# Performance work log

Measured on AMD Instinct MI355X. Metric: run time of the kernel, lower is better.

## Reference

```python
import jax, jax.numpy as jnp
import numpy as np

B, C, H, W = 8, 256, 64, 64
NH, FF, L, K = 8, 1024, 3, 64
THR = 0.5
DH = C // NH
SCALE = 1.0 / float(np.sqrt(DH))
N = H * W


def setup_inputs() -> dict:
    key = jax.random.key(0)
    ks = jax.random.split(key, 16)
    s = 0.02
    rn = lambda k, shape: (jax.random.normal(k, shape, jnp.float32) * s)
    return {
        "x": jax.random.normal(ks[0], (B, C, H, W), jnp.float32),
        "y": jax.random.normal(ks[1], (B, C, H, W), jnp.float32),
        "proj_w": rn(ks[2], (C, 2 * C)), "proj_b": rn(ks[3], (C,)),
        "sal_w": rn(ks[4], (1, C)), "sal_b": rn(ks[5], (1,)),
        "soft_w": rn(ks[6], (2, K, C)), "soft_b": rn(ks[7], (2, K)),
        "attn_in_w": rn(ks[8], (2, L, 3 * C, C)), "attn_in_b": rn(ks[9], (2, L, 3 * C)),
        "attn_out_w": rn(ks[10], (2, L, C, C)), "attn_out_b": rn(ks[11], (2, L, C)),
        "n1_g": jnp.ones((2, L, C), jnp.float32), "n1_b": jnp.zeros((2, L, C), jnp.float32),
        "ffn_w1": rn(ks[12], (2, L, FF, C)), "ffn_b1": rn(ks[13], (2, L, FF)),
        "ffn_w2": rn(ks[14], (2, L, C, FF)), "ffn_b2": rn(ks[15], (2, L, C)),
        "n2_g": jnp.ones((2, L, C), jnp.float32), "n2_b": jnp.zeros((2, L, C), jnp.float32),
    }


def _ln(t, g, b, eps=1e-5):
    m = t.mean(-1, keepdims=True)
    v = ((t - m) ** 2).mean(-1, keepdims=True)
    return (t - m) / jnp.sqrt(v + eps) * g + b


def _layers(q, kv, p, side):
    # q: [B,N,C] pixel queries, kv: [B,K,C] soft-pooled tokens
    for l in range(L):
        iw, ib = p["attn_in_w"][side, l], p["attn_in_b"][side, l]
        qq = (q @ iw[:C].T + ib[:C]).reshape(B, -1, NH, DH)
        kk = (kv @ iw[C:2 * C].T + ib[C:2 * C]).reshape(B, K, NH, DH)
        vv = (kv @ iw[2 * C:].T + ib[2 * C:]).reshape(B, K, NH, DH)
        att = jax.nn.softmax(jnp.einsum('bnhd,bkhd->bhnk', qq, kk) * SCALE, axis=-1)
        o = jnp.einsum('bhnk,bkhd->bnhd', att, vv).reshape(B, -1, C)
        o = o @ p["attn_out_w"][side, l].T + p["attn_out_b"][side, l]
        q = _ln(q + o, p["n1_g"][side, l], p["n1_b"][side, l])
        h = jax.nn.relu(q @ p["ffn_w1"][side, l].T + p["ffn_b1"][side, l])
        h = h @ p["ffn_w2"][side, l].T + p["ffn_b2"][side, l]
        q = _ln(q + h, p["n2_g"][side, l], p["n2_b"][side, l])
    return q


def _forward(x, y, proj_w, proj_b, sal_w, sal_b, soft_w, soft_b,
             attn_in_w, attn_in_b, attn_out_w, attn_out_b, n1_g, n1_b,
             ffn_w1, ffn_b1, ffn_w2, ffn_b2, n2_g, n2_b):
    p = dict(attn_in_w=attn_in_w, attn_in_b=attn_in_b, attn_out_w=attn_out_w,
             attn_out_b=attn_out_b, n1_g=n1_g, n1_b=n1_b, ffn_w1=ffn_w1,
             ffn_b1=ffn_b1, ffn_w2=ffn_w2, ffn_b2=ffn_b2, n2_g=n2_g, n2_b=n2_b)
    xc = jnp.concatenate([x, y], axis=1)                                  # [B,2C,H,W]
    feat = jnp.einsum('oc,bchw->bohw', proj_w, xc) + proj_b[None, :, None, None]
    sal = jnp.einsum('oc,bchw->bohw', sal_w, feat) + sal_b[None, :, None, None]  # [B,1,H,W]
    heat = jax.nn.sigmoid(sal)
    fg_mask = (heat >= THR).reshape(B, 1, N)
    bg_mask = (heat < 1.0 - THR).reshape(B, 1, N)
    fmap = feat.reshape(B, C, N)
    q0 = fmap.transpose(0, 2, 1)                                          # [B,N,C]
    out = fmap
    for side, hm in ((0, heat), (1, 1.0 - heat)):
        wf = feat * hm                                                    # [B,C,H,W]
        sw = (jnp.einsum('kc,bchw->bkhw', soft_w[side], wf)
              + soft_b[side][None, :, None, None]).reshape(B, K, N)       # [B,K,N]
        pool = jnp.einsum('bkn,bcn->bkc', sw, wf.reshape(B, C, N))        # [B,K,C]
        qs = _layers(q0, pool, p, side)                                   # [B,N,C]
        mask = fg_mask if side == 0 else bg_mask
        out = jnp.where(mask, qs.transpose(0, 2, 1), out)
    # per-image skip: if no fg or no bg pixels, keep original feature
    valid = fg_mask.any(axis=(1, 2)) & bg_mask.any(axis=(1, 2))           # [B]
    out = jnp.where(valid[:, None, None], out, fmap)
    return out.reshape(B, C, H, W)


def reference(x, y, proj_w, proj_b, sal_w, sal_b, soft_w, soft_b,
              attn_in_w, attn_in_b, attn_out_w, attn_out_b, n1_g, n1_b,
              ffn_w1, ffn_b1, ffn_w2, ffn_b2, n2_g, n2_b):
    return _forward(x, y, proj_w, proj_b, sal_w, sal_b, soft_w, soft_b,
                    attn_in_w, attn_in_b, attn_out_w, attn_out_b, n1_g, n1_b,
                    ffn_w1, ffn_b1, ffn_w2, ffn_b2, n2_g, n2_b)
```

## Files before the change

kernel.cpp:

```cpp
#include <hip/hip_runtime.h>
#include <stdint.h>

#define B_ 8
#define C_ 256
#define N_ 4096
#define K_ 64
#define NH_ 8
#define FF_ 1024
#define L_ 3
#define M_ (B_*N_)
#define SCALE_ 0.17677669529663687f

typedef float f32x4 __attribute__((ext_vector_type(4)));
typedef __bf16 v8bf __attribute__((ext_vector_type(8)));

__device__ __forceinline__ float b2f(unsigned short h){
  union { uint32_t u; float f; } v; v.u = ((uint32_t)h) << 16; return v.f;
}
__device__ __forceinline__ unsigned short f2b(float f){
  union { float f; uint32_t u; } v; v.f = f;
  uint32_t r = v.u + 0x7fffu + ((v.u >> 16) & 1u);
  return (unsigned short)(r >> 16);
}
__device__ __forceinline__ void gload_lds16(const void* g, void* l){
  __builtin_amdgcn_global_load_lds(
      (const __attribute__((address_space(1))) unsigned int*)g,
      (__attribute__((address_space(3))) unsigned int*)l, 16, 0, 0);
}
__device__ __forceinline__ void unpack8(uint4 v, float* o){
  o[0]=b2f((unsigned short)(v.x & 0xffff)); o[1]=b2f((unsigned short)(v.x >> 16));
  o[2]=b2f((unsigned short)(v.y & 0xffff)); o[3]=b2f((unsigned short)(v.y >> 16));
  o[4]=b2f((unsigned short)(v.z & 0xffff)); o[5]=b2f((unsigned short)(v.z >> 16));
  o[6]=b2f((unsigned short)(v.w & 0xffff)); o[7]=b2f((unsigned short)(v.w >> 16));
}

__global__ __launch_bounds__(256) void k_f32_to_bf16(const float* __restrict__ src,
                                                     unsigned short* __restrict__ dst, int n){
  int i4 = (blockIdx.x*256 + threadIdx.x)*4;
  if (i4 >= n) return;
  float4 v = *(const float4*)(src + i4);
  uint32_t p0 = (uint32_t)f2b(v.x) | ((uint32_t)f2b(v.y) << 16);
  uint32_t p1 = (uint32_t)f2b(v.z) | ((uint32_t)f2b(v.w) << 16);
  *(uint2*)(dst + i4) = make_uint2(p0, p1);
}

__global__ __launch_bounds__(256) void k_build_xcT(const float* __restrict__ x,
                                                   const float* __restrict__ y,
                                                   unsigned short* __restrict__ xcT){
  __shared__ float t[32][33];
  int b = blockIdx.z;
  int n0 = blockIdx.x*32, c0 = blockIdx.y*32;
  int tx = threadIdx.x, ty = threadIdx.y;
  const float* src = (c0 < 256) ? (x + ((size_t)b*256 + c0)*N_)
                                : (y + ((size_t)b*256 + (c0-256))*N_);
  #pragma unroll
  for (int i = 0; i < 4; i++){
    int cl = ty*4 + i;
    t[cl][tx] = src[(size_t)cl*N_ + n0 + tx];
  }
  __syncthreads();
  #pragma unroll
  for (int i = 0; i < 4; i++){
    int nl = ty*4 + i;
    xcT[((size_t)b*N_ + n0 + nl)*512 + c0 + tx] = f2b(t[tx][nl]);
  }
}

__global__ __launch_bounds__(256) void k_featmir(const float* __restrict__ featT,
                                                 unsigned short* __restrict__ featbf,
                                                 unsigned short* __restrict__ featC){
  __shared__ float t[32][33];
  int b = blockIdx.z;
  int n0 = blockIdx.x*32, c0 = blockIdx.y*32;
  int tx = threadIdx.x, ty = threadIdx.y;
  #pragma unroll
  for (int i = 0; i < 4; i++){
    int nl = ty*4 + i;
    size_t m = (size_t)b*N_ + n0 + nl;
    float v = featT[m*256 + c0 + tx];
    t[nl][tx] = v;
    featbf[m*256 + c0 + tx] = f2b(v);
  }
  __syncthreads();
  #pragma unroll
  for (int i = 0; i < 4; i++){
    int cl = ty*4 + i;
    featC[((size_t)b*256 + c0 + cl)*(size_t)N_ + n0 + tx] = f2b(t[tx][cl]);
  }
}

__global__ __launch_bounds__(512) void k_compute_u(const float* __restrict__ sal_w,
                                                   const float* __restrict__ proj_w,
                                                   const float* __restrict__ proj_b,
                                                   const float* __restrict__ sal_b,
                                                   double* __restrict__ u){
  int c2 = threadIdx.x;
// ... 84 lines not shown
      v8bf af[4], bfr[4];
      #pragma unroll
      for (int f = 0; f < 4; f++){
        int ra = wr*64 + f*16 + lr;
        int rb2 = wc*64 + f*16 + lr;
        int u = kk*4 + lk;
        af[f]  = *(const v8bf*)(&ldsA[ra*64 + ((u ^ (ra&7))<<3)]);
        bfr[f] = *(const v8bf*)(&ldsB[rb2*64 + ((u ^ (rb2&7))<<3)]);
      }
      #pragma unroll
      for (int fi = 0; fi < 4; fi++)
        #pragma unroll
        for (int fj = 0; fj < 4; fj++)
          acc[fi][fj] = __builtin_amdgcn_mfma_f32_16x16x32_bf16(af[fi], bfr[fj], acc[fi][fj], 0, 0, 0);
    }
    __syncthreads();
  }
  if (EPI == 1 || EPI == 2){
    unsigned short* st = &smem[0][0][0];
    #pragma unroll
    for (int fj = 0; fj < 4; fj++){
      int col = wc*64 + fj*16 + lr;
      float bv = bias[n0 + col];
      #pragma unroll
      for (int fi = 0; fi < 4; fi++){
        int rl = wr*64 + fi*16 + lk*4;
        #pragma unroll
        for (int r = 0; r < 4; r++){
          float v = acc[fi][fj][r] + bv;
          if (EPI == 1) v = fmaxf(v, 0.f);
          st[(rl + r)*136 + col] = f2b(v);
        }
      }
    }
    __syncthreads();
    #pragma unroll
    for (int it = 0; it < 8; it++){
      int idx = it*256 + tid;
      int row = idx >> 4, c8 = (idx & 15)*8;
      *(uint4*)((unsigned short*)out + (size_t)(m0+row)*N + n0 + c8)
          = *(const uint4*)&st[row*136 + c8];
    }
  } else {
    #pragma unroll
    for (int fj = 0; fj < 4; fj++){
      int col = n0 + wc*64 + fj*16 + lr;
      float bv = bias[col];
      #pragma unroll
      for (int fi = 0; fi < 4; fi++){
        int rb = m0 + wr*64 + fi*16 + lk*4;
        #pragma unroll
        for (int r = 0; r < 4; r++){
          float v = acc[fi][fj][r] + bv;
          if (EPI == 3){
            int row = rb + r;
            ((unsigned short*)out)[((size_t)(row>>6)*256 + col)*64 + (row&63)] = f2b(v);
          } else {
            ((float*)out)[(size_t)(rb + r)*N + col] = v;
          }
        }
      }
    }
  }
}

__global__ __launch_bounds__(256) void k_kv(
    const unsigned short* __restrict__ pool, const unsigned short* __restrict__ iw,
    const float* __restrict__ ib, unsigned short* __restrict__ kk_bf,
    unsigned short* __restrict__ vvT_bf){
  __shared__ unsigned short smem[2][2][128*64];
  int tid = threadIdx.x;
  int w = tid >> 6, l = tid & 63;
  int m0 = blockIdx.x * 128, n0 = blockIdx.y * 128;
  int isv = blockIdx.z;
  const unsigned short* W = iw + (size_t)(isv ? 512 : 256)*256;
  const float* bias = ib + (isv ? 512 : 256);
  int wr = w >> 1, wc = w & 1;
  int lr = l & 15, lk = l >> 4;
  f32x4 acc[4][4] = {};
  #pragma unroll
  for (int i = 0; i < 4; i++){
    int idx = i*256 + tid;
    int row = idx >> 3, su = ((idx & 7) ^ (row & 7))*8;
    gload_lds16(pool + (size_t)(m0+row)*256 + su, &smem[0][0][idx*8]);
    gload_lds16(W + (size_t)(n0+row)*256 + su, &smem[0][1][idx*8]);
  }
  __syncthreads();
  for (int t = 0; t < 4; ++t){
    int cur = t & 1;
    if (t + 1 < 4){
      int k0 = (t + 1) << 6;
      #pragma unroll
      for (int i = 0; i < 4; i++){
        int idx = i*256 + tid;
        int row = idx >> 3, su = ((idx & 7) ^ (row & 7))*8;
        gload_lds16(pool + (size_t)(m0+row)*256 + k0 + su, &smem[cur^1][0][idx*8]);
        gload_lds16(W + (size_t)(n0+row)*256 + k0 + su, &smem[cur^1][1][idx*8]);
      }
    }
    const unsigned short* ldsA = smem[cur][0];
    const unsigned short* ldsB = smem[cur][1];
    #pragma unroll
    for (int kk = 0; kk < 2; kk++){
      v8bf af[4], bfr[4];
      #pragma unroll
      for (int f = 0; f < 4; f++){
        int ra = wr*64 + f*16 + lr;
        int rb2 = wc*64 + f*16 + lr;
        int u = kk*4 + lk;
        af[f]  = *(const v8bf*)(&ldsA[ra*64 + ((u ^ (ra&7))<<3)]);
        bfr[f] = *(const v8bf*)(&ldsB[rb2*64 + ((u ^ (rb2&7))<<3)]);
      }
      #pragma unroll
      for (int fi = 0; fi < 4; fi++)
        #pragma unroll
        for (int fj = 0; fj < 4; fj++)
          acc[fi][fj] = __builtin_amdgcn_mfma_f32_16x16x32_bf16(af[fi], bfr[fj], acc[fi][fj], 0, 0, 0);
    }
    __syncthreads();
  }
  #pragma unroll
  for (int fj = 0; fj < 4; fj++){
    int col = n0 + wc*64 + fj*16 + lr;
    float bv = bias[col];
    #pragma unroll
    for (int fi = 0; fi < 4; fi++){
      int rb = m0 + wr*64 + fi*16 + lk*4;
      #pragma unroll
      for (int r = 0; r < 4; r++){
        float v = acc[fi][fj][r] + bv;
        int row = rb + r;
        if (isv)
          vvT_bf[((size_t)(row>>6)*256 + col)*64 + (row&63)] = f2b(v);
        else
          kk_bf[(size_t)row*256 + col] = f2b(v);
      }
    }
  }
}

template<int RF32>
__global__ __launch_bounds__(512) void k_gemm_ln(
    const unsigned short* __restrict__ A, const unsigned short* __restrict__ W,
    const float* __restrict__ bias, const void* __restrict__ resid,
    const float* __restrict__ g, const float* __restrict__ bta,
    unsigned short* __restrict__ qout){
  __shared__ unsigned short smem[49152];
  int tid = threadIdx.x;
  int w = tid >> 6, l = tid & 63;
  int m0 = blockIdx.x * 128;
  int wm = w >> 2, wf = w & 3;
  int lr = l & 15, lk = l >> 4;
  f32x4 acc[4][4] = {};
  #pragma unroll
  for (int i = 0; i < 2; i++){
    int idx = i*512 + tid;
    int row = idx >> 3, su = ((idx & 7) ^ (row & 7))*8;
    gload_lds16(A + (size_t)(m0+row)*256 + su, &smem[idx*8]);
  }
  #pragma unroll
  for (int i = 0; i < 4; i++){
    int idx = i*512 + tid;
    int row = idx >> 3, su = ((idx & 7) ^ (row & 7))*8;
    gload_lds16(W + (size_t)row*256 + su, &smem[8192 + idx*8]);
  }
  __syncthreads();
  for (int t = 0; t < 4; ++t){
    int cur = t & 1;
    if (t + 1 < 4){
      int k0 = (t + 1) << 6;
      unsigned short* bA = smem + (cur^1)*24576;
      unsigned short* bB = bA + 8192;
      #pragma unroll
      for (int i = 0; i < 2; i++){
        int idx = i*512 + tid;
        int row = idx >> 3, su = ((idx & 7) ^ (row & 7))*8;
        gload_lds16(A + (size_t)(m0+row)*256 + k0 + su, &bA[idx*8]);
      }
      #pragma unroll
      for (int i = 0; i < 4; i++){
        int idx = i*512 + tid;
        int row = idx >> 3, su = ((idx & 7) ^ (row & 7))*8;
        gload_lds16(W + (size_t)row*256 + k0 + su, &bB[idx*8]);
      }
    }
    const unsigned short* bA = smem + cur*24576;
    const unsigned short* bB = bA + 8192;
    #pragma unroll
    for (int kk = 0; kk < 2; kk++){
      v8bf af[4], wb[4];
      int u = kk*4 + lk;
      #pragma unroll
      for (int f = 0; f < 4; f++){
        int ra = wm*64 + f*16 + lr;
        af[f] = *(const v8bf*)&bA[ra*64 + ((u ^ (ra&7))<<3)];
      }
      #pragma unroll
      for (int f = 0; f < 4; f++){
        int rc = wf*64 + f*16 + lr;
        wb[f] = *(const v8bf*)&bB[rc*64 + ((u ^ (rc&7))<<3)];
      }
      #pragma unroll
      for (int fi = 0; fi < 4; fi++)
        #pragma unroll
        for (int fc = 0; fc < 4; fc++)
          acc[fi][fc] = __builtin_amdgcn_mfma_f32_16x16x32_bf16(af[fi], wb[fc], acc[fi][fc], 0, 0, 0);
    }
    __syncthreads();
  }
  unsigned short* st = smem;
  #pragma unroll
  for (int fc = 0; fc < 4; fc++){
    int col = wf*64 + fc*16 + lr;
    float bv = bias[col];
    #pragma unroll
    for (int fi = 0; fi < 4; fi++){
      int rl = wm*64 + fi*16 + lk*4;
      #pragma unroll
      for (int r = 0; r < 4; r++)
        st[(rl + r)*264 + col] = f2b(acc[fi][fc][r] + bv);
    }
  }
  __syncthreads();
  int row = tid >> 2, seg = tid & 3;
  float xv[64];
  #pragma unroll
  for (int j = 0; j < 8; j++){
    int cu = seg*8 + j;
    uint4 dv = *(const uint4*)&st[row*264 + cu*8];
    float dd[8];
    unpack8(dv, dd);
    if (RF32){
      const float* rp = (const float*)resid + (size_t)(m0+row)*256 + cu*8;
      float4 r0 = *(const float4*)rp, r1 = *(const float4*)(rp + 4);
      xv[j*8+0] = r0.x + dd[0]; xv[j*8+1] = r0.y + dd[1];
      xv[j*8+2] = r0.z + dd[2]; xv[j*8+3] = r0.w + dd[3];
      xv[j*8+4] = r1.x + dd[4]; xv[j*8+5] = r1.y + dd[5];
      xv[j*8+6] = r1.z + dd[6]; xv[j*8+7] = r1.w + dd[7];
    } else {
      uint4 rv = *(const uint4*)((const unsigned short*)resid + (size_t)(m0+row)*256 + cu*8);
      float rr[8];
      unpack8(rv, rr);
      #pragma unroll
      for (int e = 0; e < 8; e++) xv[j*8+e] = rr[e] + dd[e];
    }
  }
  float s = 0.f, q = 0.f;
  #pragma unroll
  for (int i2 = 0; i2 < 64; i2++){ s += xv[i2]; q += xv[i2]*xv[i2]; }
  s += __shfl_xor(s, 1); s += __shfl_xor(s, 2);
  q += __shfl_xor(q, 1); q += __shfl_xor(q, 2);
  float mean = s * (1.0f/256.0f);
  float rstd = 1.0f / sqrtf(q*(1.0f/256.0f) - mean*mean + 1e-5f);
  #pragma unroll
  for (int j = 0; j < 8; j++){
    int c0 = seg*64 + j*8;
    float4 g0 = *(const float4*)(g + c0), g1 = *(const float4*)(g + c0 + 4);
    float4 b0 = *(const float4*)(bta + c0), b1 = *(const float4*)(bta + c0 + 4);
    uint4 ov;
    ov.x = (uint32_t)f2b((xv[j*8+0]-mean)*rstd*g0.x + b0.x)
         | ((uint32_t)f2b((xv[j*8+1]-mean)*rstd*g0.y + b0.y) << 16);
    ov.y = (uint32_t)f2b((xv[j*8+2]-mean)*rstd*g0.z + b0.z)
         | ((uint32_t)f2b((xv[j*8+3]-mean)*rstd*g0.w + b0.w) << 16);
    ov.z = (uint32_t)f2b((xv[j*8+4]-mean)*rstd*g1.x + b1.x)
         | ((uint32_t)f2b((xv[j*8+5]-mean)*rstd*g1.y + b1.y) << 16);
    ov.w = (uint32_t)f2b((xv[j*8+6]-mean)*rstd*g1.z + b1.z)
         | ((uint32_t)f2b((xv[j*8+7]-mean)*rstd*g1.w + b1.w) << 16);
    *(uint4*)&st[row*264 + c0] = ov;
  }
  __syncthreads();
  #pragma unroll
  for (int it = 0; it < 8; it++){
    int idx = it*512 + tid;
    int rw = idx >> 5, c8 = (idx & 31)*8;
    *(uint4*)(qout + (size_t)(m0+rw)*256 + c8) = *(const uint4*)&st[rw*264 + c8];
  }
}

__global__ __launch_bounds__(512) void k_ffn(
    const unsigned short* __restrict__ qb, const unsigned short* __restrict__ W1g,
    const float* __restrict__ b1g, const unsigned short* __restrict__ W2g,
    const float* __restrict__ b2g, unsigned short* __restrict__ outb){
  __shared__ unsigned short smem[73728];
  unsigned short* sA  = smem;
  unsigned short* sW1 = smem + 32768;
  unsigned short* sW2 = smem + 49152;
  unsigned short* sH  = smem + 65536;
  int tid = threadIdx.x;
  int w = tid >> 6, l = tid & 63;
  int m0 = blockIdx.x * 128;
  int wm = w >> 2;
  int wf = w & 3;
  int lr = l & 15, lk = l >> 4;

  #pragma unroll
  for (int i = 0; i < 8; i++){
    int idx = i*512 + tid;
    int row = idx >> 5, g = idx & 31;
    int su = (g & 24) | ((g & 7) ^ (row & 7));
    gload_lds16(qb + (size_t)(m0+row)*256 + su*8, &sA[idx*8]);
  }
  #pragma unroll
  for (int i = 0; i < 4; i++){
    int idx = i*512 + tid;
    int row = idx >> 5, g = idx & 31;
    int su = (g & 24) | ((g & 7) ^ (row & 7));
    gload_lds16(W1g + (size_t)row*256 + su*8, &sW1[idx*8]);
  }
  #pragma unroll
  for (int i = 0; i < 4; i++){
    int idx = i*512 + tid;
    int row = idx >> 3, g = idx & 7;
    int su = g ^ (row & 7);
    gload_lds16(W2g + (size_t)row*1024 + su*8, &sW2[idx*8]);
  }
  __syncthreads();

  f32x4 acc[4][4] = {};
  for (int cc = 0; cc < 16; ++cc){
    f32x4 hacc[4] = {};
    #pragma unroll
    for (int ks = 0; ks < 8; ks++){
      int g = ks*4 + lk;
      int rf = wf*16 + lr;
      v8bf bf1 = *(const v8bf*)&sW1[rf*256 + (((g & 24) | ((g & 7) ^ (rf & 7)))<<3)];
      #pragma unroll
      for (int f = 0; f < 4; f++){
        int ra = wm*64 + f*16 + lr;
        v8bf af = *(const v8bf*)&sA[ra*256 + (((g & 24) | ((g & 7) ^ (ra & 7)))<<3)];
        hacc[f] = __builtin_amdgcn_mfma_f32_16x16x32_bf16(af, bf1, hacc[f], 0, 0, 0);
      }
    }
    {
      int fc = wf*16 + lr;
      float b1v = b1g[cc*64 + fc];
      #pragma unroll
      for (int fi = 0; fi < 4; fi++){
        int mr0 = wm*64 + fi*16 + lk*4;
        #pragma unroll
        for (int r = 0; r < 4; r++){
          float v = fmaxf(hacc[fi][r] + b1v, 0.f);
          int mr = mr0 + r;
          sH[mr*64 + (((fc >> 3) ^ (mr & 7))<<3) + (fc & 7)] = f2b(v);
        }
      }
// ... 126 lines not shown
    }
    #pragma unroll
    for (int i = 0; i < 4; i++){
      int idx = i*256 + tid;
      int row = idx >> 3, su = (idx & 7) ^ (row & 7);
      gload_lds16(W + (size_t)row*4096 + k0 + su*8, &ldsB[idx*8]);
    }
    __syncthreads();
    #pragma unroll
    for (int kk = 0; kk < 2; kk++){
      v8bf af[4], bfr[4];
      #pragma unroll
      for (int f = 0; f < 4; f++){
        int ra = wr*64 + f*16 + lr;
        int rb2 = wc*64 + f*16 + lr;
        int u = kk*4 + lk;
        af[f]  = *(const v8bf*)(&ldsA[ra*64 + ((u ^ (ra&7))<<3)]);
        bfr[f] = *(const v8bf*)(&ldsB[rb2*64 + ((u ^ (rb2&7))<<3)]);
      }
      #pragma unroll
      for (int fi = 0; fi < 4; fi++)
        #pragma unroll
        for (int fj = 0; fj < 4; fj++)
          acc[fi][fj] = __builtin_amdgcn_mfma_f32_16x16x32_bf16(af[fi], bfr[fj], acc[fi][fj], 0, 0, 0);
    }
    __syncthreads();
  }
  float* dst = pp + ((size_t)kc*8 + b)*128*256;
  #pragma unroll
  for (int fj = 0; fj < 4; fj++){
    int col = nt*128 + wc*64 + fj*16 + lr;
    #pragma unroll
    for (int fi = 0; fi < 4; fi++){
      int rb = wr*64 + fi*16 + lk*4;
      #pragma unroll
      for (int r = 0; r < 4; r++)
        dst[(size_t)(rb + r)*256 + col] = acc[fi][fj][r];
    }
  }
}

__global__ __launch_bounds__(256) void k_pool2b(const float* __restrict__ pp,
                                                unsigned short* __restrict__ pool_bf_s){
  int bk = blockIdx.x, side = blockIdx.y, c = threadIdx.x;
  int b = bk >> 6, k = bk & 63;
  float s = 0.f;
  #pragma unroll
  for (int kc = 0; kc < 8; kc++)
    s += pp[(((size_t)kc*8 + b)*128 + side*64 + k)*256 + c];
  pool_bf_s[((size_t)side*512 + bk)*256 + c] = f2b(s);
}

__global__ __launch_bounds__(256) void k_attn2(
    const unsigned short* __restrict__ qq, const unsigned short* __restrict__ kk,
    const unsigned short* __restrict__ vvT, unsigned short* __restrict__ obf){
  __shared__ unsigned short sk[64*256];
  __shared__ unsigned short svT[256*64];
  __shared__ unsigned short sp[4][16*64];
  __shared__ unsigned short sow[4][16*32];
  int tid = threadIdx.x, w = tid >> 6, l = tid & 63;
  int blk = blockIdx.x, b = blk >> 6;
  int l15 = l & 15, lg = l >> 4;
  const uint4* ksrc = (const uint4*)(kk + (size_t)b*64*256);
  #pragma unroll
  for (int i = 0; i < 8; i++){
    int u = i*256 + tid;
    int row = u >> 5, j = u & 31;
    *(uint4*)&sk[row*256 + ((j ^ (row&7))<<3)] = ksrc[u];
  }
  const uint4* vsrc = (const uint4*)(vvT + (size_t)b*256*64);
  #pragma unroll
  for (int i = 0; i < 8; i++){
    int u = i*256 + tid;
    int row = u >> 3, j = u & 7;
    *(uint4*)&svT[row*64 + ((j ^ (row&7))<<3)] = vsrc[u];
  }
  __syncthreads();
  size_t qrow = (size_t)blk*64 + w*16 + l15;
  for (int h = 0; h < 8; h++){
    v8bf aq = *(const v8bf*)(qq + qrow*256 + h*32 + lg*8);
    f32x4 s[4];
    #pragma unroll
    for (int kt = 0; kt < 4; kt++){
      int row = kt*16 + l15;
      v8bf bk = *(const v8bf*)&sk[row*256 + (((h*4 + lg) ^ (row&7))<<3)];
      f32x4 z = {};
      s[kt] = __builtin_amdgcn_mfma_f32_16x16x32_bf16(aq, bk, z, 0, 0, 0);
    }
    #pragma unroll
    for (int r = 0; r < 4; r++){
      float v0 = s[0][r]*SCALE_, v1 = s[1][r]*SCALE_;
      float v2 = s[2][r]*SCALE_, v3 = s[3][r]*SCALE_;
      float mx = fmaxf(fmaxf(v0, v1), fmaxf(v2, v3));
      mx = fmaxf(mx, __shfl_xor(mx, 1));
      mx = fmaxf(mx, __shfl_xor(mx, 2));
      mx = fmaxf(mx, __shfl_xor(mx, 4));
      mx = fmaxf(mx, __shfl_xor(mx, 8));
      float e0 = __expf(v0-mx), e1 = __expf(v1-mx);
      float e2 = __expf(v2-mx), e3 = __expf(v3-mx);
      float sum = e0+e1+e2+e3;
      sum += __shfl_xor(sum, 1); sum += __shfl_xor(sum, 2);
      sum += __shfl_xor(sum, 4); sum += __shfl_xor(sum, 8);
      float inv = 1.0f/sum;
      s[0][r] = e0*inv; s[1][r] = e1*inv; s[2][r] = e2*inv; s[3][r] = e3*inv;
    }
    #pragma unroll
    for (int kt = 0; kt < 4; kt++){
      int colu = kt*2 + (l15>>3);
      #pragma unroll
      for (int r = 0; r < 4; r++){
        int row = lg*4 + r;
        sp[w][row*64 + ((colu ^ (row&7))<<3) + (l&7)] = f2b(s[kt][r]);
      }
    }
    f32x4 o[2] = {};
    #pragma unroll
    for (int k2 = 0; k2 < 2; k2++){
      v8bf pa = *(const v8bf*)&sp[w][l15*64 + (((k2*4 + lg) ^ (l15&7))<<3)];
      #pragma unroll
      for (int dt = 0; dt < 2; dt++){
        int vrow = h*32 + dt*16 + l15;
        v8bf bv = *(const v8bf*)&svT[vrow*64 + (((k2*4 + lg) ^ (vrow&7))<<3)];
        o[dt] = __builtin_amdgcn_mfma_f32_16x16x32_bf16(pa, bv, o[dt], 0, 0, 0);
      }
    }
    #pragma unroll
    for (int dt = 0; dt < 2; dt++)
      #pragma unroll
      for (int r = 0; r < 4; r++)
        sow[w][(lg*4 + r)*32 + dt*16 + l15] = f2b(o[dt][r]);
    uint4 ov = *(const uint4*)&sow[w][l15*32 + lg*8];
    *(uint4*)(obf + qrow*256 + h*32 + lg*8) = ov;
  }
}

template<int RF32>
__global__ __launch_bounds__(256) void k_ln2(
    const void* __restrict__ resid, const unsigned short* __restrict__ delta,
    const float* __restrict__ g, const float* __restrict__ bta,
    unsigned short* __restrict__ qout){
  int wv = threadIdx.x >> 6, l = threadIdx.x & 63;
  size_t m = (size_t)blockIdx.x*4 + wv;
  uint2 dv = *(const uint2*)(delta + m*256 + l*4);
  float d0 = b2f((unsigned short)(dv.x & 0xffff)), d1 = b2f((unsigned short)(dv.x >> 16));
  float d2 = b2f((unsigned short)(dv.y & 0xffff)), d3 = b2f((unsigned short)(dv.y >> 16));
  float x0, x1, x2, x3;
  if (RF32){
    float4 rv = *(const float4*)((const float*)resid + m*256 + l*4);
    x0 = rv.x+d0; x1 = rv.y+d1; x2 = rv.z+d2; x3 = rv.w+d3;
  } else {
    uint2 rv = *(const uint2*)((const unsigned short*)resid + m*256 + l*4);
    x0 = b2f((unsigned short)(rv.x & 0xffff)) + d0;
    x1 = b2f((unsigned short)(rv.x >> 16)) + d1;
    x2 = b2f((unsigned short)(rv.y & 0xffff)) + d2;
    x3 = b2f((unsigned short)(rv.y >> 16)) + d3;
  }
  float s = x0+x1+x2+x3;
  float ss = x0*x0+x1*x1+x2*x2+x3*x3;
  #pragma unroll
  for (int off = 32; off; off >>= 1){
    s  += __shfl_xor(s, off);
    ss += __shfl_xor(ss, off);
  }
  float mean = s * (1.0f/256.0f);
  float var = ss * (1.0f/256.0f) - mean*mean;
  float rstd = 1.0f / sqrtf(var + 1e-5f);
  float4 gv = *(const float4*)(g + l*4);
  float4 bv = *(const float4*)(bta + l*4);
  float y0 = (x0-mean)*rstd*gv.x + bv.x;
  float y1 = (x1-mean)*rstd*gv.y + bv.y;
  float y2 = (x2-mean)*rstd*gv.z + bv.z;
  float y3 = (x3-mean)*rstd*gv.w + bv.w;
  uint32_t p0 = (uint32_t)f2b(y0) | ((uint32_t)f2b(y1)<<16);
  uint32_t p1 = (uint32_t)f2b(y2) | ((uint32_t)f2b(y3)<<16);
  *(uint2*)(qout + m*256 + l*4) = make_uint2(p0,p1);
}

__global__ __launch_bounds__(256) void k_select(
    const unsigned short* __restrict__ qA, const unsigned short* __restrict__ qB,
    const float* __restrict__ featT, const float* __restrict__ heat,
    const int* __restrict__ counts, float* __restrict__ out){
  __shared__ float t[32][33];
  int b = blockIdx.z;
  int n0 = blockIdx.x*32, c0 = blockIdx.y*32;
  int tx = threadIdx.x, ty = threadIdx.y;
  bool valid = (counts[b*2] > 0) && (counts[b*2+1] > 0);
  #pragma unroll
  for (int i = 0; i < 4; i++){
    int nl = ty*4+i;
    size_t m = (size_t)b*4096 + n0 + nl;
    float v;
    if (!valid) v = featT[m*256 + c0 + tx];
    else {
      bool fg = heat[(size_t)b*4096 + n0 + nl] >= 0.5f;
      v = fg ? b2f(qA[m*256 + c0 + tx]) : b2f(qB[m*256 + c0 + tx]);
    }
    t[nl][tx] = v;
  }
  __syncthreads();
  #pragma unroll
  for (int i = 0; i < 4; i++){
    int cl = ty*4+i;
    out[((size_t)b*256 + c0 + cl)*4096 + n0 + tx] = t[tx][cl];
  }
}

extern "C" void kernel_launch(void* const* d_in, const int* in_sizes, int n_in,
                              void* d_out, int out_size, void* d_ws, size_t ws_size,
                              hipStream_t stream){
  const float* x         = (const float*)d_in[0];
  const float* y         = (const float*)d_in[1];
  const float* proj_w    = (const float*)d_in[2];
  const float* proj_b    = (const float*)d_in[3];
  const float* sal_w     = (const float*)d_in[4];
  const float* sal_b     = (const float*)d_in[5];
  const float* soft_w    = (const float*)d_in[6];
  const float* soft_b    = (const float*)d_in[7];
  const float* attn_in_w = (const float*)d_in[8];
  const float* attn_in_b = (const float*)d_in[9];
  const float* attn_out_w= (const float*)d_in[10];
  const float* attn_out_b= (const float*)d_in[11];
  const float* n1_g      = (const float*)d_in[12];
  const float* n1_b      = (const float*)d_in[13];
  const float* ffn_w1    = (const float*)d_in[14];
  const float* ffn_b1    = (const float*)d_in[15];
  const float* ffn_w2    = (const float*)d_in[16];
  const float* ffn_b2    = (const float*)d_in[17];
  const float* n2_g      = (const float*)d_in[18];
  const float* n2_b      = (const float*)d_in[19];
  float* out = (float*)d_out;

  char* p = (char*)d_ws;
  auto alloc = [&](size_t bytes){ char* r = p; p += (bytes + 255) & ~(size_t)255; return r; };
  unsigned short* hbf   = (unsigned short*)alloc((size_t)M_*FF_*2);
  unsigned short* xcT   = hbf;
  unsigned short* qq_bf = hbf;
  float* featT = (float*)alloc((size_t)M_*C_*4);
  unsigned short* qAb = (unsigned short*)alloc((size_t)M_*C_*2);
  unsigned short* swh = qAb;
  unsigned short* qBb = (unsigned short*)alloc((size_t)M_*C_*2);
  unsigned short* obf = (unsigned short*)alloc((size_t)M_*C_*2);
  unsigned short* featC = obf;
  unsigned short* featbf = (unsigned short*)alloc((size_t)M_*C_*2);
  unsigned short* tmpb = (unsigned short*)alloc((size_t)M_*C_*2);
  float* g_all = (float*)tmpb;
  float* pp    = (float*)alloc((size_t)8*8*128*256*4);
  double* salp = (double*)pp;
  unsigned short* pool_bf_s = (unsigned short*)alloc((size_t)2*512*256*2);
  unsigned short* kk_bf = (unsigned short*)alloc((size_t)B_*K_*C_*2);
  unsigned short* vvT_bf= (unsigned short*)alloc((size_t)B_*C_*K_*2);
  float* heat = (float*)alloc((size_t)B_*N_*4);
  double* u   = (double*)alloc(513*8);
  int* counts = (int*)alloc(64);
  float* zbias = (float*)alloc(512);
  unsigned short* projw_bf = (unsigned short*)alloc((size_t)C_*512*2);
  unsigned short* aiw_bf = (unsigned short*)alloc((size_t)2*L_*768*C_*2);
  unsigned short* aow_bf = (unsigned short*)alloc((size_t)2*L_*C_*C_*2);
  unsigned short* f1w_bf = (unsigned short*)alloc((size_t)2*L_*FF_*C_*2);
  unsigned short* f2w_bf = (unsigned short*)alloc((size_t)2*L_*C_*FF_*2);
  unsigned short* sw2_bf = (unsigned short*)alloc((size_t)2*K_*C_*2);

  hipMemsetAsync(counts, 0, 64, stream);
  hipMemsetAsync(zbias, 0, 512, stream);
  k_compute_u<<<1, 512, 0, stream>>>(sal_w, proj_w, proj_b, sal_b, u);
  k_sal_part<<<dim3(128, 16), 256, 0, stream>>>(x, y, u, salp);
  k_sal_red<<<128, 256, 0, stream>>>(salp, u, heat, counts);

  auto conv = [&](const float* s, unsigned short* d, size_t n){
    k_f32_to_bf16<<<(unsigned)((n/4 + 255)/256), 256, 0, stream>>>(s, d, (int)n);
  };
  conv(proj_w,     projw_bf, (size_t)C_*512);
  conv(attn_in_w,  aiw_bf,   (size_t)2*L_*768*C_);
  conv(attn_out_w, aow_bf,   (size_t)2*L_*C_*C_);
  conv(ffn_w1,     f1w_bf,   (size_t)2*L_*FF_*C_);
  conv(ffn_w2,     f2w_bf,   (size_t)2*L_*C_*FF_);
  conv(soft_w,     sw2_bf,   (size_t)2*K_*C_);

  k_build_xcT<<<dim3(N_/32, 512/32, B_), dim3(32,8), 0, stream>>>(x, y, xcT);
  k_gemm_bt<0><<<dim3(M_/128, C_/128), 256, 0, stream>>>(xcT, projw_bf, proj_b, featT, M_, C_, 512);
  k_featmir<<<dim3(N_/32, C_/32, B_), dim3(32,8), 0, stream>>>(featT, featbf, featC);

  k_gemm_bt<0><<<dim3(M_/128, 1), 256, 0, stream>>>(featbf, sw2_bf, zbias, g_all, M_, 128, C_);
  k_swh<<<M_/64, 256, 0, stream>>>(g_all, heat, soft_b, swh);
  k_poolgemm<<<dim3(8, 2, B_), 256, 0, stream>>>(swh, featC, pp);
  k_pool2b<<<dim3(512, 2), 256, 0, stream>>>(pp, pool_bf_s);

  for (int side = 0; side < 2; ++side){
    unsigned short* qb = side ? qBb : qAb;
    const unsigned short* poolS = pool_bf_s + (size_t)side*512*256;
    for (int lyr = 0; lyr < L_; ++lyr){
      int sl = side*L_ + lyr;
      const unsigned short* iw = aiw_bf + (size_t)sl*768*C_;
      const float* ib = attn_in_b + (size_t)sl*768;
      const unsigned short* qin = (lyr == 0) ? featbf : qb;
      k_gemm_bt<2><<<dim3(M_/128, C_/128), 256, 0, stream>>>(qin, iw, ib, qq_bf, M_, C_, C_);
      k_kv<<<dim3(4, 2, 2), 256, 0, stream>>>(poolS, iw, ib, kk_bf, vvT_bf);
      k_attn2<<<M_/64, 256, 0, stream>>>(qq_bf, kk_bf, vvT_bf, obf);
      if (lyr == 0)
        k_gemm_ln<1><<<M_/128, 512, 0, stream>>>(obf, aow_bf + (size_t)sl*C_*C_,
            attn_out_b + (size_t)sl*C_, featT, n1_g + (size_t)sl*C_, n1_b + (size_t)sl*C_, qb);
      else
        k_gemm_ln<0><<<M_/128, 512, 0, stream>>>(obf, aow_bf + (size_t)sl*C_*C_,
            attn_out_b + (size_t)sl*C_, qb, n1_g + (size_t)sl*C_, n1_b + (size_t)sl*C_, qb);
      k_ffn<<<M_/128, 512, 0, stream>>>(qb, f1w_bf + (size_t)sl*FF_*C_, ffn_b1 + (size_t)sl*FF_,
                                        f2w_bf + (size_t)sl*C_*FF_, ffn_b2 + (size_t)sl*C_, tmpb);
      k_ln2<0><<<M_/4, 256, 0, stream>>>(qb, tmpb, n2_g + (size_t)sl*C_, n2_b + (size_t)sl*C_, qb);
    }
  }
  k_select<<<dim3(N_/32, C_/32, B_), dim3(32,8), 0, stream>>>(qAb, qBb, featT, heat, counts, out);
}
```

Before: 875.4 us.

## Batch both sides into single launches and fuse Q/K/V projections

Processes the fg and bg transformer stacks together by doubling the row dimension, so each layer launches one kernel per stage covering both sides, with per-block selection of the right weights. The Q projection and the K/V projections are merged into one k_qkv kernel. The six weight conversions become one launch. This roughly halves the number of kernel launches and gives each launch a larger grid, which should help occupancy on the small K/V and attention kernels. The cost is larger workspace buffers.

```diff
diff --git a/kernel.cpp b/kernel.cpp
--- a/kernel.cpp
+++ b/kernel.cpp
@@ -9,6 +9,7 @@
 #define FF_ 1024
 #define L_ 3
 #define M_ (B_*N_)
+#define M2_ (2*M_)
 #define SCALE_ 0.17677669529663687f
 
 typedef float f32x4 __attribute__((ext_vector_type(4)));
@@ -34,14 +35,28 @@
   o[6]=b2f((unsigned short)(v.w & 0xffff)); o[7]=b2f((unsigned short)(v.w >> 16));
 }
 
-__global__ __launch_bounds__(256) void k_f32_to_bf16(const float* __restrict__ src,
-                                                     unsigned short* __restrict__ dst, int n){
+__global__ __launch_bounds__(256) void k_convall(
+    const float* s0, unsigned short* d0, int n0_,
+    const float* s1, unsigned short* d1, int n1_,
+    const float* s2, unsigned short* d2, int n2_,
+    const float* s3, unsigned short* d3, int n3_,
+    const float* s4, unsigned short* d4, int n4_,
+    const float* s5, unsigned short* d5, int n5_){
+  const float* s; unsigned short* d; int n;
+  switch (blockIdx.y){
+    case 0: s=s0; d=d0; n=n0_; break;
+    case 1: s=s1; d=d1; n=n1_; break;
+    case 2: s=s2; d=d2; n=n2_; break;
+    case 3: s=s3; d=d3; n=n3_; break;
+    case 4: s=s4; d=d4; n=n4_; break;
+    default:s=s5; d=d5; n=n5_; break;
+  }
   int i4 = (blockIdx.x*256 + threadIdx.x)*4;
   if (i4 >= n) return;
-  float4 v = *(const float4*)(src + i4);
+  float4 v = *(const float4*)(s + i4);
   uint32_t p0 = (uint32_t)f2b(v.x) | ((uint32_t)f2b(v.y) << 16);
   uint32_t p1 = (uint32_t)f2b(v.z) | ((uint32_t)f2b(v.w) << 16);
-  *(uint2*)(dst + i4) = make_uint2(p0, p1);
+  *(uint2*)(d + i4) = make_uint2(p0, p1);
 }
 
 __global__ __launch_bounds__(256) void k_build_xcT(const float* __restrict__ x,
@@ -232,37 +247,56 @@
         #pragma unroll
         for (int r = 0; r < 4; r++){
           float v = acc[fi][fj][r] + bv;
-          if (EPI == 3){
-            int row = rb + r;
-            ((unsigned short*)out)[((size_t)(row>>6)*256 + col)*64 + (row&63)] = f2b(v);
-          } else {
-            ((float*)out)[(size_t)(rb + r)*N + col] = v;
-          }
+          ((float*)out)[(size_t)(rb + r)*N + col] = v;
         }
       }
     }
   }
 }
 
-__global__ __launch_bounds__(256) void k_kv(
-    const unsigned short* __restrict__ pool, const unsigned short* __restrict__ iw,
-    const float* __restrict__ ib, unsigned short* __restrict__ kk_bf,
-    unsigned short* __restrict__ vvT_bf){
+__global__ __launch_bounds__(256) void k_qkv(
+    const unsigned short* __restrict__ qin0, const unsigned short* __restrict__ qin1,
+    const unsigned short* __restrict__ pool2, const unsigned short* __restrict__ aiw,
+    const float* __restrict__ aib, int sl0,
+    unsigned short* __restrict__ qq2, unsigned short* __restrict__ kk2,
+    unsigned short* __restrict__ vvT2){
   __shared__ unsigned short smem[2][2][128*64];
   int tid = threadIdx.x;
   int w = tid >> 6, l = tid & 63;
-  int m0 = blockIdx.x * 128, n0 = blockIdx.y * 128;
-  int isv = blockIdx.z;
-  const unsigned short* W = iw + (size_t)(isv ? 512 : 256)*256;
-  const float* bias = ib + (isv ? 512 : 256);
+  int bx = blockIdx.x, n0 = blockIdx.y*128;
   int wr = w >> 1, wc = w & 1;
   int lr = l & 15, lk = l >> 4;
+  const unsigned short* Aptr; size_t abase;
+  const unsigned short* W; const float* bias;
+  int mode, m0;
+  if (bx < 512){
+    mode = 0; m0 = bx*128;
+    int side = (m0 >= M_) ? 1 : 0;
+    Aptr = side ? qin1 : qin0; abase = (size_t)(m0 - side*M_);
+    int sl = sl0 + side*L_;
+    W = aiw + (size_t)sl*768*C_;
+    bias = aib + (size_t)sl*768;
+  } else if (bx < 520){
+    mode = 1; m0 = (bx - 512)*128;
+    int side = (m0 >= 512) ? 1 : 0;
+    Aptr = pool2; abase = (size_t)m0;
+    int sl = sl0 + side*L_;
+    W = aiw + (size_t)sl*768*C_ + (size_t)256*C_;
+    bias = aib + (size_t)sl*768 + 256;
+  } else {
+    mode = 2; m0 = (bx - 520)*128;
+    int side = (m0 >= 512) ? 1 : 0;
+    Aptr = pool2; abase = (size_t)m0;
+    int sl = sl0 + side*L_;
+    W = aiw + (size_t)sl*768*C_ + (size_t)512*C_;
+    bias = aib + (size_t)sl*768 + 512;
+  }
   f32x4 acc[4][4] = {};
   #pragma unroll
   for (int i = 0; i < 4; i++){
     int idx = i*256 + tid;
     int row = idx >> 3, su = ((idx & 7) ^ (row & 7))*8;
-    gload_lds16(pool + (size_t)(m0+row)*256 + su, &smem[0][0][idx*8]);
+    gload_lds16(Aptr + (abase+row)*256 + su, &smem[0][0][idx*8]);
     gload_lds16(W + (size_t)(n0+row)*256 + su, &smem[0][1][idx*8]);
   }
   __syncthreads();
@@ -274,7 +308,7 @@
       for (int i = 0; i < 4; i++){
         int idx = i*256 + tid;
         int row = idx >> 3, su = ((idx & 7) ^ (row & 7))*8;
-        gload_lds16(pool + (size_t)(m0+row)*256 + k0 + su, &smem[cur^1][0][idx*8]);
+        gload_lds16(Aptr + (abase+row)*256 + k0 + su, &smem[cur^1][0][idx*8]);
         gload_lds16(W + (size_t)(n0+row)*256 + k0 + su, &smem[cur^1][1][idx*8]);
       }
     }
@@ -299,36 +333,65 @@
     }
     __syncthreads();
   }
-  #pragma unroll
-  for (int fj = 0; fj < 4; fj++){
-    int col = n0 + wc*64 + fj*16 + lr;
-    float bv = bias[col];
-    #pragma unroll
-    for (int fi = 0; fi < 4; fi++){
-      int rb = m0 + wr*64 + fi*16 + lk*4;
-      #pragma unroll
-      for (int r = 0; r < 4; r++){
-        float v = acc[fi][fj][r] + bv;
-        int row = rb + r;
-        if (isv)
-          vvT_bf[((size_t)(row>>6)*256 + col)*64 + (row&63)] = f2b(v);
-        else
-          kk_bf[(size_t)row*256 + col] = f2b(v);
-      }
+  if (mode == 2){
+    int side = (m0 >= 512) ? 1 : 0;
+    #pragma unroll
+    for (int fj = 0; fj < 4; fj++){
+      int col = n0 + wc*64 + fj*16 + lr;
+      float bv = bias[col];
+      #pragma unroll
+      for (int fi = 0; fi < 4; fi++){
+        int rb = m0 + wr*64 + fi*16 + lk*4;
+        #pragma unroll
+        for (int r = 0; r < 4; r++){
+          float v = acc[fi][fj][r] + bv;
+          int rl = rb + r - side*512;
+          vvT2[(size_t)side*(B_*C_*K_) + ((size_t)(rl>>6)*256 + col)*64 + (rl&63)] = f2b(v);
+        }
+      }
+    }
+  } else {
+    unsigned short* outp = (mode == 0) ? qq2 : kk2;
+    unsigned short* st = &smem[0][0][0];
+    #pragma unroll
+    for (int fj = 0; fj < 4; fj++){
+      int col = wc*64 + fj*16 + lr;
+      float bv = bias[n0 + col];
+      #pragma unroll
+      for (int fi = 0; fi < 4; fi++){
+        int rl = wr*64 + fi*16 + lk*4;
+        #pragma unroll
+        for (int r = 0; r < 4; r++)
+          st[(rl + r)*136 + col] = f2b(acc[fi][fj][r] + bv);
+      }
+    }
+    __syncthreads();
+    #pragma unroll
+    for (int it = 0; it < 8; it++){
+      int idx = it*256 + tid;
+      int row = idx >> 4, c8 = (idx & 15)*8;
+      *(uint4*)(outp + (size_t)(m0+row)*256 + n0 + c8) = *(const uint4*)&st[row*136 + c8];
     }
   }
 }
 
 template<int RF32>
 __global__ __launch_bounds__(512) void k_gemm_ln(
-    const unsigned short* __restrict__ A, const unsigned short* __restrict__ W,
-    const float* __restrict__ bias, const void* __restrict__ resid,
-    const float* __restrict__ g, const float* __restrict__ bta,
+    const unsigned short* __restrict__ A, const unsigned short* __restrict__ aow,
+    const float* __restrict__ aob, const void* __restrict__ resid,
+    const float* __restrict__ n1g, const float* __restrict__ n1b, int sl0,
     unsigned short* __restrict__ qout){
   __shared__ unsigned short smem[49152];
   int tid = threadIdx.x;
   int w = tid >> 6, l = tid & 63;
   int m0 = blockIdx.x * 128;
+  int side = (m0 >= M_) ? 1 : 0;
+  int sl = sl0 + side*L_;
+  const unsigned short* W = aow + (size_t)sl*C_*C_;
+  const float* bias = aob + (size_t)sl*C_;
+  const float* g = n1g + (size_t)sl*C_;
+  const float* bta = n1b + (size_t)sl*C_;
+  size_t rbase = RF32 ? (size_t)(m0 - side*M_) : (size_t)m0;
   int wm = w >> 2, wf = w & 3;
   int lr = l & 15, lk = l >> 4;
   f32x4 acc[4][4] = {};
@@ -411,14 +474,14 @@
     float dd[8];
     unpack8(dv, dd);
     if (RF32){
-      const float* rp = (const float*)resid + (size_t)(m0+row)*256 + cu*8;
+      const float* rp = (const float*)resid + (rbase+row)*256 + cu*8;
       float4 r0 = *(const float4*)rp, r1 = *(const float4*)(rp + 4);
       xv[j*8+0] = r0.x + dd[0]; xv[j*8+1] = r0.y + dd[1];
       xv[j*8+2] = r0.z + dd[2]; xv[j*8+3] = r0.w + dd[3];
       xv[j*8+4] = r1.x + dd[4]; xv[j*8+5] = r1.y + dd[5];
       xv[j*8+6] = r1.z + dd[6]; xv[j*8+7] = r1.w + dd[7];
     } else {
-      uint4 rv = *(const uint4*)((const unsigned short*)resid + (size_t)(m0+row)*256 + cu*8);
+      uint4 rv = *(const uint4*)((const unsigned short*)resid + (rbase+row)*256 + cu*8);
       float rr[8];
       unpack8(rv, rr);
       #pragma unroll
@@ -458,9 +521,9 @@
 }
 
 __global__ __launch_bounds__(512) void k_ffn(
-    const unsigned short* __restrict__ qb, const unsigned short* __restrict__ W1g,
-    const float* __restrict__ b1g, const unsigned short* __restrict__ W2g,
-    const float* __restrict__ b2g, unsigned short* __restrict__ outb){
+    const unsigned short* __restrict__ qb, const unsigned short* __restrict__ f1w,
+    const float* __restrict__ f1b, const unsigned short* __restrict__ f2w,
+    const float* __restrict__ f2b_, int sl0, unsigned short* __restrict__ outb){
   __shared__ unsigned short smem[73728];
   unsigned short* sA  = smem;
   unsigned short* sW1 = smem + 32768;
@@ -469,8 +532,13 @@
   int tid = threadIdx.x;
   int w = tid >> 6, l = tid & 63;
   int m0 = blockIdx.x * 128;
-  int wm = w >> 2;
-  int wf = w & 3;
+  int side = (m0 >= M_) ? 1 : 0;
+  int sl = sl0 + side*L_;
+  const unsigned short* W1g = f1w + (size_t)sl*FF_*C_;
+  const float* b1g = f1b + (size_t)sl*FF_;
+  const unsigned short* W2g = f2w + (size_t)sl*C_*FF_;
+  const float* b2g = f2b_ + (size_t)sl*C_;
+  int wm = w >> 2, wf = w & 3;
   int lr = l & 15, lk = l >> 4;
 
   #pragma unroll
@@ -703,23 +771,26 @@
 }
 
 __global__ __launch_bounds__(256) void k_attn2(
-    const unsigned short* __restrict__ qq, const unsigned short* __restrict__ kk,
-    const unsigned short* __restrict__ vvT, unsigned short* __restrict__ obf){
+    const unsigned short* __restrict__ qq2, const unsigned short* __restrict__ kk2,
+    const unsigned short* __restrict__ vvT2, unsigned short* __restrict__ obf2){
   __shared__ unsigned short sk[64*256];
   __shared__ unsigned short svT[256*64];
   __shared__ unsigned short sp[4][16*64];
   __shared__ unsigned short sow[4][16*32];
   int tid = threadIdx.x, w = tid >> 6, l = tid & 63;
-  int blk = blockIdx.x, b = blk >> 6;
+  int blk = blockIdx.x;
+  int side = (blk >= 512) ? 1 : 0;
+  int lblk = blk - side*512;
+  int b = lblk >> 6;
   int l15 = l & 15, lg = l >> 4;
-  const uint4* ksrc = (const uint4*)(kk + (size_t)b*64*256);
+  const uint4* ksrc = (const uint4*)(kk2 + ((size_t)side*512 + (size_t)b*64)*256);
   #pragma unroll
   for (int i = 0; i < 8; i++){
     int u = i*256 + tid;
     int row = u >> 5, j = u & 31;
     *(uint4*)&sk[row*256 + ((j ^ (row&7))<<3)] = ksrc[u];
   }
-  const uint4* vsrc = (const uint4*)(vvT + (size_t)b*256*64);
+  const uint4* vsrc = (const uint4*)(vvT2 + ((size_t)side*B_ + b)*256*64);
   #pragma unroll
   for (int i = 0; i < 8; i++){
     int u = i*256 + tid;
@@ -729,7 +800,7 @@
   __syncthreads();
   size_t qrow = (size_t)blk*64 + w*16 + l15;
   for (int h = 0; h < 8; h++){
-    v8bf aq = *(const v8bf*)(qq + qrow*256 + h*32 + lg*8);
+    v8bf aq = *(const v8bf*)(qq2 + qrow*256 + h*32 + lg*8);
     f32x4 s[4];
     #pragma unroll
     for (int kt = 0; kt < 4; kt++){
@@ -781,31 +852,27 @@
       for (int r = 0; r < 4; r++)
         sow[w][(lg*4 + r)*32 + dt*16 + l15] = f2b(o[dt][r]);
     uint4 ov = *(const uint4*)&sow[w][l15*32 + lg*8];
-    *(uint4*)(obf + qrow*256 + h*32 + lg*8) = ov;
-  }
-}
-
-template<int RF32>
+    *(uint4*)(obf2 + qrow*256 + h*32 + lg*8) = ov;
+  }
+}
+
 __global__ __launch_bounds__(256) void k_ln2(
-    const void* __restrict__ resid, const unsigned short* __restrict__ delta,
-    const float* __restrict__ g, const float* __restrict__ bta,
+    const unsigned short* __restrict__ resid, const unsigned short* __restrict__ delta,
+    const float* __restrict__ n2g, const float* __restrict__ n2b, int sl0,
     unsigned short* __restrict__ qout){
   int wv = threadIdx.x >> 6, l = threadIdx.x & 63;
   size_t m = (size_t)blockIdx.x*4 + wv;
+  int side = (m >= (size_t)M_) ? 1 : 0;
+  const float* g = n2g + (size_t)(sl0 + side*L_)*C_;
+  const float* bta = n2b + (size_t)(sl0 + side*L_)*C_;
   uint2 dv = *(const uint2*)(delta + m*256 + l*4);
   float d0 = b2f((unsigned short)(dv.x & 0xffff)), d1 = b2f((unsigned short)(dv.x >> 16));
   float d2 = b2f((unsigned short)(dv.y & 0xffff)), d3 = b2f((unsigned short)(dv.y >> 16));
-  float x0, x1, x2, x3;
-  if (RF32){
-    float4 rv = *(const float4*)((const float*)resid + m*256 + l*4);
-    x0 = rv.x+d0; x1 = rv.y+d1; x2 = rv.z+d2; x3 = rv.w+d3;
-  } else {
-    uint2 rv = *(const uint2*)((const unsigned short*)resid + m*256 + l*4);
-    x0 = b2f((unsigned short)(rv.x & 0xffff)) + d0;
-    x1 = b2f((unsigned short)(rv.x >> 16)) + d1;
-    x2 = b2f((unsigned short)(rv.y & 0xffff)) + d2;
-    x3 = b2f((unsigned short)(rv.y >> 16)) + d3;
-  }
+  uint2 rv = *(const uint2*)(resid + m*256 + l*4);
+  float x0 = b2f((unsigned short)(rv.x & 0xffff)) + d0;
+  float x1 = b2f((unsigned short)(rv.x >> 16)) + d1;
+  float x2 = b2f((unsigned short)(rv.y & 0xffff)) + d2;
+  float x3 = b2f((unsigned short)(rv.y >> 16)) + d3;
   float s = x0+x1+x2+x3;
   float ss = x0*x0+x1*x1+x2*x2+x3*x3;
   #pragma unroll
@@ -883,32 +950,31 @@
 
   char* p = (char*)d_ws;
   auto alloc = [&](size_t bytes){ char* r = p; p += (bytes + 255) & ~(size_t)255; return r; };
-  unsigned short* hbf   = (unsigned short*)alloc((size_t)M_*FF_*2);
-  unsigned short* xcT   = hbf;
-  unsigned short* qq_bf = hbf;
+  unsigned short* big0 = (unsigned short*)alloc((size_t)M2_*C_*2);
+  unsigned short* xcT  = big0;
+  unsigned short* qq2  = big0;
   float* featT = (float*)alloc((size_t)M_*C_*4);
-  unsigned short* qAb = (unsigned short*)alloc((size_t)M_*C_*2);
-  unsigned short* swh = qAb;
-  unsigned short* qBb = (unsigned short*)alloc((size_t)M_*C_*2);
-  unsigned short* obf = (unsigned short*)alloc((size_t)M_*C_*2);
-  unsigned short* featC = obf;
+  unsigned short* q2   = (unsigned short*)alloc((size_t)M2_*C_*2);
+  unsigned short* swh  = q2;
+  unsigned short* obf2 = (unsigned short*)alloc((size_t)M2_*C_*2);
+  unsigned short* featC = obf2;
   unsigned short* featbf = (unsigned short*)alloc((size_t)M_*C_*2);
-  unsigned short* tmpb = (unsigned short*)alloc((size_t)M_*C_*2);
-  float* g_all = (float*)tmpb;
+  unsigned short* tmpb2 = (unsigned short*)alloc((size_t)M2_*C_*2);
+  float* g_all = (float*)tmpb2;
   float* pp    = (float*)alloc((size_t)8*8*128*256*4);
   double* salp = (double*)pp;
   unsigned short* pool_bf_s = (unsigned short*)alloc((size_t)2*512*256*2);
-  unsigned short* kk_bf = (unsigned short*)alloc((size_t)B_*K_*C_*2);
-  unsigned short* vvT_bf= (unsigned short*)alloc((size_t)B_*C_*K_*2);
+  unsigned short* kk2  = (unsigned short*)alloc((size_t)2*B_*K_*C_*2);
+  unsigned short* vvT2 = (unsigned short*)alloc((size_t)2*B_*C_*K_*2);
   float* heat = (float*)alloc((size_t)B_*N_*4);
   double* u   = (double*)alloc(513*8);
   int* counts = (int*)alloc(64);
   float* zbias = (float*)alloc(512);
   unsigned short* projw_bf = (unsigned short*)alloc((size_t)C_*512*2);
   unsigned short* aiw_bf = (unsigned short*)alloc((size_t)2*L_*768*C_*2);
-  unsigned short* aow_bf = (unsigned short*)alloc((size_t)2*L_*C_*C_*2);
   unsigned short* f1w_bf = (unsigned short*)alloc((size_t)2*L_*FF_*C_*2);
   unsigned short* f2w_bf = (unsigned short*)alloc((size_t)2*L_*C_*FF_*2);
+  unsigned short* aow_bf = (unsigned short*)alloc((size_t)2*L_*C_*C_*2);
   unsigned short* sw2_bf = (unsigned short*)alloc((size_t)2*K_*C_*2);
 
   hipMemsetAsync(counts, 0, 64, stream);
@@ -917,15 +983,16 @@
   k_sal_part<<<dim3(128, 16), 256, 0, stream>>>(x, y, u, salp);
   k_sal_red<<<128, 256, 0, stream>>>(salp, u, heat, counts);
 
-  auto conv = [&](const float* s, unsigned short* d, size_t n){
-    k_f32_to_bf16<<<(unsigned)((n/4 + 255)/256), 256, 0, stream>>>(s, d, (int)n);
-  };
-  conv(proj_w,     projw_bf, (size_t)C_*512);
-  conv(attn_in_w,  aiw_bf,   (size_t)2*L_*768*C_);
-  conv(attn_out_w, aow_bf,   (size_t)2*L_*C_*C_);
-  conv(ffn_w1,     f1w_bf,   (size_t)2*L_*FF_*C_);
-  conv(ffn_w2,     f2w_bf,   (size_t)2*L_*C_*FF_);
-  conv(soft_w,     sw2_bf,   (size_t)2*K_*C_);
+  {
+    int n0c = (int)((size_t)2*L_*FF_*C_);
+    k_convall<<<dim3((unsigned)((n0c/4 + 255)/256), 6), 256, 0, stream>>>(
+        ffn_w1, f1w_bf, n0c,
+        ffn_w2, f2w_bf, (int)((size_t)2*L_*C_*FF_),
+        attn_in_w, aiw_bf, (int)((size_t)2*L_*768*C_),
+        attn_out_w, aow_bf, (int)((size_t)2*L_*C_*C_),
+        proj_w, projw_bf, (int)((size_t)C_*512),
+        soft_w, sw2_bf, (int)((size_t)2*K_*C_));
+  }
 
   k_build_xcT<<<dim3(N_/32, 512/32, B_), dim3(32,8), 0, stream>>>(x, y, xcT);
   k_gemm_bt<0><<<dim3(M_/128, C_/128), 256, 0, stream>>>(xcT, projw_bf, proj_b, featT, M_, C_, 512);
@@ -936,27 +1003,18 @@
   k_poolgemm<<<dim3(8, 2, B_), 256, 0, stream>>>(swh, featC, pp);
   k_pool2b<<<dim3(512, 2), 256, 0, stream>>>(pp, pool_bf_s);
 
-  for (int side = 0; side < 2; ++side){
-    unsigned short* qb = side ? qBb : qAb;
-    const unsigned short* poolS = pool_bf_s + (size_t)side*512*256;
-    for (int lyr = 0; lyr < L_; ++lyr){
-      int sl = side*L_ + lyr;
-      const unsigned short* iw = aiw_bf + (size_t)sl*768*C_;
-      const float* ib = attn_in_b + (size_t)sl*768;
-      const unsigned short* qin = (lyr == 0) ? featbf : qb;
-      k_gemm_bt<2><<<dim3(M_/128, C_/128), 256, 0, stream>>>(qin, iw, ib, qq_bf, M_, C_, C_);
-      k_kv<<<dim3(4, 2, 2), 256, 0, stream>>>(poolS, iw, ib, kk_bf, vvT_bf);
-      k_attn2<<<M_/64, 256, 0, stream>>>(qq_bf, kk_bf, vvT_bf, obf);
-      if (lyr == 0)
-        k_gemm_ln<1><<<M_/128, 512, 0, stream>>>(obf, aow_bf + (size_t)sl*C_*C_,
-            attn_out_b + (size_t)sl*C_, featT, n1_g + (size_t)sl*C_, n1_b + (size_t)sl*C_, qb);
-      else
-        k_gemm_ln<0><<<M_/128, 512, 0, stream>>>(obf, aow_bf + (size_t)sl*C_*C_,
-            attn_out_b + (size_t)sl*C_, qb, n1_g + (size_t)sl*C_, n1_b + (size_t)sl*C_, qb);
-      k_ffn<<<M_/128, 512, 0, stream>>>(qb, f1w_bf + (size_t)sl*FF_*C_, ffn_b1 + (size_t)sl*FF_,
-                                        f2w_bf + (size_t)sl*C_*FF_, ffn_b2 + (size_t)sl*C_, tmpb);
-      k_ln2<0><<<M_/4, 256, 0, stream>>>(qb, tmpb, n2_g + (size_t)sl*C_, n2_b + (size_t)sl*C_, qb);
-    }
-  }
-  k_select<<<dim3(N_/32, C_/32, B_), dim3(32,8), 0, stream>>>(qAb, qBb, featT, heat, counts, out);
-}
+  for (int lyr = 0; lyr < L_; ++lyr){
+    const unsigned short* qin0 = (lyr == 0) ? featbf : q2;
+    const unsigned short* qin1 = (lyr == 0) ? featbf : (q2 + (size_t)M_*C_);
+    k_qkv<<<dim3(528, 2), 256, 0, stream>>>(qin0, qin1, pool_bf_s, aiw_bf, attn_in_b, lyr,
+                                            qq2, kk2, vvT2);
+    k_attn2<<<1024, 256, 0, stream>>>(qq2, kk2, vvT2, obf2);
+    if (lyr == 0)
+      k_gemm_ln<1><<<512, 512, 0, stream>>>(obf2, aow_bf, attn_out_b, featT, n1_g, n1_b, lyr, q2);
+    else
+      k_gemm_ln<0><<<512, 512, 0, stream>>>(obf2, aow_bf, attn_out_b, q2, n1_g, n1_b, lyr, q2);
+    k_ffn<<<512, 512, 0, stream>>>(q2, f1w_bf, ffn_b1, f2w_bf, ffn_b2, lyr, tmpb2);
+    k_ln2<<<M2_/4, 256, 0, stream>>>(q2, tmpb2, n2_g, n2_b, lyr, q2);
+  }
+  k_select<<<dim3(N_/32, C_/32, B_), dim3(32,8), 0, stream>>>(q2, q2 + (size_t)M_*C_, featT, heat, counts, out);
+}
```

Measured after the change: 783.8 us (median of 3 runs). 10.5% less time.
